# Performance work log

Hardware: AMD Instinct MI355X
Metric: run time of the kernel (lower is better)

## Reference

```python
import jax, jax.numpy as jnp
import numpy as np

B, TT, TA, H = 2, 128, 512, 1024
EPS = 1e-5


def _conv1d(x, w, b, pad):
    # x: [B, C_in, T], w: [C_out, C_in, K] -> [B, C_out, T]
    y = jax.lax.conv_general_dilated(x, w, window_strides=(1,), padding=[(pad, pad)],
                                     dimension_numbers=('NCH', 'OIH', 'NCH'))
    return y + b[None, :, None]


def _groupnorm1(x, g, b):
    # GroupNorm(num_groups=1): normalize over (C, T) per sample. x: [B, C, T]
    mu = jnp.mean(x, axis=(1, 2), keepdims=True)
    var = jnp.var(x, axis=(1, 2), keepdims=True)
    xn = (x - mu) * jax.lax.rsqrt(var + EPS)
    return xn * g[None, :, None] + b[None, :, None]


def setup_inputs() -> dict:
    key = jax.random.key(0)
    ks = jax.random.split(key, 16)
    s = 0.02
    return {
        'text_hidden': jax.random.normal(ks[0], (B, TT, H), jnp.float32),
        'audio_hidden': jax.random.normal(ks[1], (B, TA, H), jnp.float32),
        # alignment_proj: Linear(2H, H) -> ReLU -> Linear(H, 1)
        'a_w1': jax.random.normal(ks[2], (2 * H, H), jnp.float32) * s,
        'a_b1': jnp.zeros((H,), jnp.float32),
        'a_w2': jax.random.normal(ks[3], (H, 1), jnp.float32) * s,
        'a_b2': jnp.zeros((1,), jnp.float32),
        # duration_predictor: Conv1d(H,H,3) ReLU GN(1,H) Conv1d(H,H,3) ReLU GN(1,H) Conv1d(H,1,1)
        'd_w1': jax.random.normal(ks[4], (H, H, 3), jnp.float32) * s,
        'd_b1': jnp.zeros((H,), jnp.float32),
        'gn1_g': jnp.ones((H,), jnp.float32),
        'gn1_b': jnp.zeros((H,), jnp.float32),
        'd_w2': jax.random.normal(ks[5], (H, H, 3), jnp.float32) * s,
        'd_b2': jnp.zeros((H,), jnp.float32),
        'gn2_g': jnp.ones((H,), jnp.float32),
        'gn2_b': jnp.zeros((H,), jnp.float32),
        'd_w3': jax.random.normal(ks[6], (1, H, 1), jnp.float32) * s,
        'd_b3': jnp.zeros((1,), jnp.float32),
    }


def reference(text_hidden, audio_hidden, a_w1, a_b1, a_w2, a_b2,
              d_w1, d_b1, gn1_g, gn1_b, d_w2, d_b2, gn2_g, gn2_b, d_w3, d_b3):
    # ---- predict_durations ----
    x = jnp.swapaxes(text_hidden, 1, 2)                      # [B, H, TT]
    x = _groupnorm1(jax.nn.relu(_conv1d(x, d_w1, d_b1, 1)), gn1_g, gn1_b)
    x = _groupnorm1(jax.nn.relu(_conv1d(x, d_w2, d_b2, 1)), gn2_g, gn2_b)
    x = _conv1d(x, d_w3, d_b3, 0)                            # [B, 1, TT]
    durations = jax.nn.softplus(x[:, 0, :])                  # [B, TT]

    # ---- soft_mas (temperature = 1.0) ----
    # Linear on concat([text, audio]) == text @ W1[:H] + audio @ W1[H:] + b1
    t_part = jnp.einsum('bth,hd->btd', text_hidden, a_w1[:H])    # [B, TT, H]
    a_part = jnp.einsum('bah,hd->bad', audio_hidden, a_w1[H:])   # [B, TA, H]
    hid = jax.nn.relu(t_part[:, :, None, :] + a_part[:, None, :, :] + a_b1)  # [B,TT,TA,H]
    logits = jnp.einsum('btad,do->bta', hid, a_w2) + a_b2[0]     # [B, TT, TA]

    pos = jnp.arange(TA, dtype=logits.dtype)                     # audio positions j
    expected = jnp.arange(TT, dtype=logits.dtype) * (TA / TT)    # expected pos per text i
    monotonic_bias = -0.1 * jnp.abs(pos[None, :] - expected[:, None])  # [TT, TA]
    logits = logits + monotonic_bias[None, :, :]

    alignment = jax.nn.softmax(logits, axis=-1)
    return alignment, durations
```

## Files before the change

kernel.cpp:

```cpp
#include <hip/hip_runtime.h>
#include <hip/hip_bf16.h>


typedef __bf16 bf16_t;
typedef __bf16 bf16x8 __attribute__((ext_vector_type(8)));
typedef __bf16 bf16x4 __attribute__((ext_vector_type(4)));
typedef float  f32x4  __attribute__((ext_vector_type(4)));
typedef _Float16 f16_t;
typedef _Float16 f16x2 __attribute__((ext_vector_type(2)));
typedef _Float16 f16x4 __attribute__((ext_vector_type(4)));

#define EPSV 1e-5f

#define OFF_TEXTBF   0u
#define OFF_AUDIOBF  524288u
#define OFF_W1TOP    2621440u
#define OFF_W1BOT    4718592u
#define OFF_WC1      6815744u
#define OFF_WC2      13107200u
#define OFF_TP       19398656u
#define OFF_W2F      19922944u
#define OFF_APT      20447232u
#define OFF_XP0      22544384u
#define OFF_XP1      23076864u
#define OFF_Y2       23609344u
#define OFF_BST1     24133632u
#define OFF_BST2     24137728u
#define OFF_LP       24141824u

__global__ __launch_bounds__(256) void prep_k(
    const float* __restrict__ text, const float* __restrict__ audio,
    const float* __restrict__ w1,
    const float* __restrict__ w1c, const float* __restrict__ w2c,
    const float* __restrict__ w2,
    bf16_t* __restrict__ text_bf, bf16_t* __restrict__ xp0,
    bf16_t* __restrict__ audio_bf,
    bf16_t* __restrict__ topT, bf16_t* __restrict__ botT,
    bf16_t* __restrict__ wc1, bf16_t* __restrict__ wc2,
    bf16_t* __restrict__ xp1, f16_t* __restrict__ w2f)
{
    __shared__ float tile[32][33];
    const int bid = blockIdx.x;
    if (bid < 1280) {
        const int e = (bid * 256 + threadIdx.x) * 4;
        if (e < 262144) {
            float4 v = *(const float4*)&text[e];
            bf16x4 o; o[0] = (bf16_t)v.x; o[1] = (bf16_t)v.y; o[2] = (bf16_t)v.z; o[3] = (bf16_t)v.w;
            *(bf16x4*)&text_bf[e] = o;
            const int bt = e >> 10, h = e & 1023;
            const int b = bt >> 7, t = bt & 127;
            *(bf16x4*)&xp0[(size_t)(b * 130 + 1 + t) * 1024 + h] = o;
        } else {
            const int ea = e - 262144;
            float4 v = *(const float4*)&audio[ea];
            bf16x4 o; o[0] = (bf16_t)v.x; o[1] = (bf16_t)v.y; o[2] = (bf16_t)v.z; o[3] = (bf16_t)v.w;
            *(bf16x4*)&audio_bf[ea] = o;
        }
    } else if (bid < 3328) {
        const int b2 = bid - 1280;
        const int bx = b2 & 31, by = b2 >> 5;
        const int tx = threadIdx.x & 31, ty = threadIdx.x >> 5;
        #pragma unroll
        for (int j = 0; j < 4; ++j)
            tile[ty + j * 8][tx] = w1[(size_t)(by * 32 + ty + j * 8) * 1024 + bx * 32 + tx];
        __syncthreads();
        bf16_t* out = (by < 32) ? topT : botT;
        const int hbase = (by & 31) * 32;
        #pragma unroll
        for (int j = 0; j < 4; ++j) {
            const int d = bx * 32 + ty + j * 8;
            out[(size_t)d * 1024 + hbase + tx] = (bf16_t)tile[tx][ty + j * 8];
        }
    } else if (bid < 5376) {
        int b2 = bid - 3328;
        const float* w = (b2 < 1024) ? w1c : w2c;
        bf16_t* wc = (b2 < 1024) ? wc1 : wc2;
        b2 &= 1023;
        const int t = b2 * 256 + threadIdx.x;
        const int o = t >> 8, i4 = t & 255;
        const float* src = w + (size_t)o * 3072 + i4 * 12;
        float4 v0 = *(const float4*)&src[0];
        float4 v1 = *(const float4*)&src[4];
        float4 v2 = *(const float4*)&src[8];
        const float f[12] = {v0.x, v0.y, v0.z, v0.w, v1.x, v1.y, v1.z, v1.w, v2.x, v2.y, v2.z, v2.w};
        #pragma unroll
        for (int r = 0; r < 3; ++r) {
            bf16x4 o4;
            #pragma unroll
            for (int j = 0; j < 4; ++j) o4[j] = (bf16_t)f[j * 3 + r];
            *(bf16x4*)&wc[(size_t)r * 1048576 + (size_t)o * 1024 + i4 * 4] = o4;
        }
    } else {
        const int tid = threadIdx.x;
        const int rowmap[4] = {0, 129, 130, 259};
        const int f = tid * 16;
        const int r = f >> 10, w = f & 1023;
        bf16x8 z8 = (bf16x8)(bf16_t)0.0f;
        bf16_t* p0 = xp0 + (size_t)rowmap[r] * 1024 + w;
        bf16_t* p1 = xp1 + (size_t)rowmap[r] * 1024 + w;
        *(bf16x8*)p0 = z8; *(bf16x8*)(p0 + 8) = z8;
        *(bf16x8*)p1 = z8; *(bf16x8*)(p1 + 8) = z8;
        float4 wv = *(const float4*)&w2[tid * 4];
        f16x4 wo; wo[0] = (f16_t)wv.x; wo[1] = (f16_t)wv.y; wo[2] = (f16_t)wv.z; wo[3] = (f16_t)wv.w;
        *(f16x4*)&w2f[tid * 4] = wo;
    }
}

__device__ __forceinline__ void conv_tile(
    const bf16_t* __restrict__ Wc, const bf16_t* __restrict__ xp,
    const float* __restrict__ bias, bf16_t* __restrict__ out,
    int rowsPerB, int rowOff, float* __restrict__ bstat, int statIdx,
    int bx, int by, int tid, float* smem, float* sred, float* sredq)
{
    const int w = tid >> 6, l = tid & 63;
    const int bt0 = bx * 32, m0 = by * 16;
    const int i0 = w * 128;
    const int lm = l & 15, lk = (l >> 4) * 8;
    const int b = bt0 >> 7, tbase = bt0 & 127;
    f32x4 acc0 = (f32x4)(0.0f), acc1 = (f32x4)(0.0f);
    const bf16_t* aq = Wc + (size_t)(m0 + lm) * 1024 + i0 + lk;
    const bf16_t* bq = xp + (size_t)(b * 130 + tbase + lm) * 1024 + i0 + lk;
    #pragma unroll
    for (int r = 0; r < 3; ++r) {
        const bf16_t* ar = aq + (size_t)r * 1048576;
        const bf16_t* br = bq + (size_t)r * 1024;
        #pragma unroll
        for (int kk = 0; kk < 128; kk += 32) {
            bf16x8 af = *(const bf16x8*)(ar + kk);
            bf16x8 bf0 = *(const bf16x8*)(br + kk);
            bf16x8 bf1 = *(const bf16x8*)(br + 16384 + kk);
            acc0 = __builtin_amdgcn_mfma_f32_16x16x32_bf16(af, bf0, acc0, 0, 0, 0);
            acc1 = __builtin_amdgcn_mfma_f32_16x16x32_bf16(af, bf1, acc1, 0, 0, 0);
        }
    }
    {
        const int row = (l >> 4) * 4;
        #pragma unroll
        for (int r = 0; r < 4; ++r) {
            smem[w * 576 + (row + r) * 36 + lm] = acc0[r];
            smem[w * 576 + (row + r) * 36 + 16 + lm] = acc1[r];
        }
    }
    __syncthreads();
    const int m = tid >> 5, n = tid & 31;
    float v = 0.f;
    #pragma unroll
    for (int ww = 0; ww < 8; ++ww) v += smem[ww * 576 + m * 36 + n];
    v = fmaxf(v + bias[m0 + m], 0.f);
    float s = v, q = v * v;
    __syncthreads();
    smem[m * 36 + n] = v;
    #pragma unroll
    for (int off = 32; off > 0; off >>= 1) {
        s += __shfl_xor(s, off);
        q += __shfl_xor(q, off);
    }
    if (l == 0) { sred[w] = s; sredq[w] = q; }
    __syncthreads();
    if (tid == 0) {
        float ts = 0.f, tq = 0.f;
        #pragma unroll
        for (int ww = 0; ww < 8; ++ww) { ts += sred[ww]; tq += sredq[ww]; }
        bstat[statIdx * 2] = ts;
        bstat[statIdx * 2 + 1] = tq;
    }
    if (tid < 64) {
        const int row = tid >> 1, half = tid & 1;
        bf16x8 o8;
        #pragma unroll
        for (int j = 0; j < 8; ++j) o8[j] = (bf16_t)smem[(half * 8 + j) * 36 + row];
        const int t = tbase + row;
        *(bf16x8*)&out[(size_t)(b * rowsPerB + rowOff + t) * 1024 + m0 + half * 8] = o8;
    }
}

__device__ __forceinline__ void reduce_bstat(
    const float* __restrict__ bstat, int b, int tid,
    float* sr, float* sq, float& mu, float& rsig)
{
    const int lane = tid & 63, wid = tid >> 6;
    float s = 0.f, q = 0.f;
    if (tid < 256) {
        float2 v = ((const float2*)bstat)[b * 256 + tid];
        s = v.x; q = v.y;
    }
    #pragma unroll
    for (int off = 32; off > 0; off >>= 1) {
        s += __shfl_xor(s, off);
        q += __shfl_xor(q, off);
    }
    if (lane == 0) { sr[wid] = s; sq[wid] = q; }
    __syncthreads();
    float ts = 0.f, tq = 0.f;
    #pragma unroll
    for (int i = 0; i < 8; ++i) { ts += sr[i]; tq += sq[i]; }
    const float cnt = 131072.f;
    mu = ts / cnt;
    const float var = tq / cnt - mu * mu;
    rsig = rsqrtf(var + EPSV);
}

__device__ __forceinline__ void gemm_unit(
    int unit, int ut, float* base,
    const bf16_t* __restrict__ text_bf, const bf16_t* __restrict__ w1topT,
    const float* __restrict__ b1, f16_t* __restrict__ tp,
    const bf16_t* __restrict__ audio_bf, const bf16_t* __restrict__ w1botT,
    f16_t* __restrict__ apT4)
{
    const int is_tp = (unit < 256) ? 1 : 0;
    const int b2 = is_tp ? unit : unit - 256;
    const int n0 = (b2 & 31) * 32, m0 = (b2 >> 5) * 32;
    const int w = ut >> 6, l = ut & 63;
    const int lm = l & 15, lk = (l >> 4) * 8;
    const int k0 = w * 256;
    const bf16_t* A  = is_tp ? text_bf : audio_bf;
    const bf16_t* Bt = is_tp ? w1topT : w1botT;
    f32x4 acc[2][2];
    #pragma unroll
    for (int mt = 0; mt < 2; ++mt)
        #pragma unroll
        for (int nt = 0; nt < 2; ++nt) acc[mt][nt] = (f32x4)(0.0f);
    const bf16_t* Ap = A + (size_t)(m0 + lm) * 1024 + k0 + lk;
    const bf16_t* Bp = Bt + (size_t)(n0 + lm) * 1024 + k0 + lk;
    #pragma unroll
    for (int kk = 0; kk < 256; kk += 32) {
        bf16x8 af[2], bfr[2];
        #pragma unroll
        for (int i = 0; i < 2; ++i) af[i] = *(const bf16x8*)(Ap + (size_t)i * 16384 + kk);
        #pragma unroll
        for (int i = 0; i < 2; ++i) bfr[i] = *(const bf16x8*)(Bp + (size_t)i * 16384 + kk);
        #pragma unroll
        for (int mt = 0; mt < 2; ++mt)
            #pragma unroll
            for (int nt = 0; nt < 2; ++nt)
                acc[mt][nt] = __builtin_amdgcn_mfma_f32_16x16x32_bf16(af[mt], bfr[nt], acc[mt][nt], 0, 0, 0);
    }
    #pragma unroll
    for (int mt = 0; mt < 2; ++mt) {
        const int row = mt * 16 + (l >> 4) * 4;
        #pragma unroll
        for (int nt = 0; nt < 2; ++nt)
            #pragma unroll
            for (int r = 0; r < 4; ++r)
                base[w * 1152 + (row + r) * 36 + nt * 16 + lm] = acc[mt][nt][r];
    }
    __syncthreads();
    if (is_tp) {
        const int m = ut >> 3, n4 = (ut & 7) * 4;
        f16x4 v;
        #pragma unroll
        for (int j = 0; j < 4; ++j)
            v[j] = (f16_t)(base[m * 36 + n4 + j] + base[1152 + m * 36 + n4 + j]
                         + base[2304 + m * 36 + n4 + j] + base[3456 + m * 36 + n4 + j]
                         + b1[n0 + n4 + j]);
        *(f16x4*)&tp[(size_t)(m0 + m) * 1024 + n0 + n4] = v;
    } else {
        const int a = ut >> 3, q = ut & 7;
        const int b = m0 >> 9, a0 = m0 & 511;
        f16x4 v;
        #pragma unroll
        for (int c = 0; c < 4; ++c)
            v[c] = (f16_t)(base[a * 36 + q * 4 + c] + base[1152 + a * 36 + q * 4 + c]
                         + base[2304 + a * 36 + q * 4 + c] + base[3456 + a * 36 + q * 4 + c]);
        const size_t hq = (size_t)(n0 >> 2) + q;
        *(f16x4*)&apT4[(hq * 1024 + b * 512 + a0 + a) * 4] = v;
    }
}

__global__ __launch_bounds__(512, 4) void p2_k(
    const bf16_t* __restrict__ wc1, const bf16_t* __restrict__ xp0,
    const float* __restrict__ d_b1, bf16_t* __restrict__ xp1,
    float* __restrict__ bstat1,
    const bf16_t* __restrict__ text_bf, const bf16_t* __restrict__ w1topT,
    const float* __restrict__ a_b1, f16_t* __restrict__ tp,
    const bf16_t* __restrict__ audio_bf, const bf16_t* __restrict__ w1botT,
    f16_t* __restrict__ apT4)
{
    __shared__ float smem[9216];
    __shared__ float sred[8], sredq[8];
    const int bid = blockIdx.x;
    const int tid = threadIdx.x;
    if (bid < 512) {
        conv_tile(wc1, xp0, d_b1, xp1, 130, 1, bstat1, bid,
                  bid >> 6, bid & 63, tid, smem, sred, sredq);
    } else {
        const int unit = (bid - 512) * 2 + (tid >> 8);
        gemm_unit(unit, tid & 255, smem + (tid >> 8) * 4608,
                  text_bf, w1topT, a_b1, tp, audio_bf, w1botT, apT4);
    }
}

__device__ __forceinline__ float dot2_acc(f16x2 x, f16x2 w, float acc) {
#if __has_builtin(__builtin_amdgcn_fdot2)
    return __builtin_amdgcn_fdot2(x, w, acc, false);
#else
    return acc + (float)x[0] * (float)w[0] + (float)x[1] * (float)w[1];
#endif
}

__global__ __launch_bounds__(512) void p3_k(
    const f16_t* __restrict__ tp, const f16_t* __restrict__ apT4,
    const f16_t* __restrict__ w2f, float* __restrict__ lp,
    bf16_t* __restrict__ xp1, const float* __restrict__ bstat1,
    const float* __restrict__ g, const float* __restrict__ bet)
{
    __shared__ float sr[8], sq[8];
    const int bid = blockIdx.x;
    const int tid = threadIdx.x;
    if (bid < 256) {
        const int btp = bid & 63, hc = bid >> 6;
        const int bt0 = btp * 4;
        const int b = bt0 >> 7;
        const int a = tid;
        const f16_t* tpr = tp + (size_t)bt0 * 1024 + hc * 256;
        const f16_t* w2r = w2f + hc * 256;
        const f16_t* apc = apT4 + ((size_t)(hc * 64) * 1024 + b * 512 + a) * 4;
        float acc[4] = {0.f, 0.f, 0.f, 0.f};
        const f16x2 zero = (f16x2)(f16_t)0.0f;
        #pragma unroll 2
        for (int hq = 0; hq < 64; hq += 2) {
            f16x4 a0 = *(const f16x4*)(apc + (size_t)hq * 4096);
            f16x4 a1 = *(const f16x4*)(apc + (size_t)(hq + 1) * 4096);
            f16x4 w0 = *(const f16x4*)&w2r[hq * 4];
            f16x4 w1 = *(const f16x4*)&w2r[hq * 4 + 4];
            #pragma unroll
            for (int r = 0; r < 4; ++r) {
                f16x4 t0 = *(const f16x4*)&tpr[r * 1024 + hq * 4];
                f16x4 t1 = *(const f16x4*)&tpr[r * 1024 + hq * 4 + 4];
                f16x2 p;
                p = __builtin_elementwise_max((f16x2){t0[0] + a0[0], t0[1] + a0[1]}, zero);
                acc[r] = dot2_acc(p, (f16x2){w0[0], w0[1]}, acc[r]);
                p = __builtin_elementwise_max((f16x2){t0[2] + a0[2], t0[3] + a0[3]}, zero);
                acc[r] = dot2_acc(p, (f16x2){w0[2], w0[3]}, acc[r]);
                p = __builtin_elementwise_max((f16x2){t1[0] + a1[0], t1[1] + a1[1]}, zero);
                acc[r] = dot2_acc(p, (f16x2){w1[0], w1[1]}, acc[r]);
                p = __builtin_elementwise_max((f16x2){t1[2] + a1[2], t1[3] + a1[3]}, zero);
                acc[r] = dot2_acc(p, (f16x2){w1[2], w1[3]}, acc[r]);
            }
        }
        float* dst = lp + (size_t)(hc * 256 + bt0) * 512 + a;
        #pragma unroll
        for (int r = 0; r < 4; ++r) dst[(size_t)r * 512] = acc[r];
    } else {
        const int gb = bid - 256;
        const int b = (gb * 2) >> 7;
        float mu, rsig;
        reduce_bstat(bstat1, b, tid, sr, sq, mu, rsig);
        const int idx4 = gb * 512 + tid;
        const int e = idx4 * 4;
        const int bt = e >> 10, o = e & 1023;
        const int t = bt & 127;
        bf16_t* p = xp1 + (size_t)(b * 130 + 1 + t) * 1024 + o;
        bf16x4 v = *(bf16x4*)p;
        float4 gv = *(const float4*)&g[o];
        float4 bv = *(const float4*)&bet[o];
        bf16x4 ov;
        ov[0] = (bf16_t)(((float)v[0] - mu) * rsig * gv.x + bv.x);
        ov[1] = (bf16_t)(((float)v[1] - mu) * rsig * gv.y + bv.y);
        ov[2] = (bf16_t)(((float)v[2] - mu) * rsig * gv.z + bv.z);
        ov[3] = (bf16_t)(((float)v[3] - mu) * rsig * gv.w + bv.w);
        *(bf16x4*)p = ov;
    }
}

__global__ __launch_bounds__(512, 4) void conv2_k(
    const bf16_t* __restrict__ wc2, const bf16_t* __restrict__ xp1,
    const float* __restrict__ d_b2, bf16_t* __restrict__ y2,
    float* __restrict__ bstat2)
{
    __shared__ float smem[4608];
    __shared__ float sred[8], sredq[8];
    conv_tile(wc2, xp1, d_b2, y2, 128, 0, bstat2, blockIdx.x,
              blockIdx.x >> 6, blockIdx.x & 63, threadIdx.x, smem, sred, sredq);
}

__global__ __launch_bounds__(512) void combine_k(
    const float* __restrict__ lp, const float* __restrict__ b2,
    const bf16_t* __restrict__ y2, const float* __restrict__ bstat2,
    const float* __restrict__ g, const float* __restrict__ bet,
    const float* __restrict__ w3, const float* __restrict__ b3,
    float* __restrict__ out)
{
    __shared__ float redm[8], redsum[8];
    const int bid = blockIdx.x;
    const int tid = threadIdx.x;
    if (bid < 256) {
        const int bt = bid, t = bt & 127;
        const int a = tid;
        const int lane = a & 63, wid = a >> 6;
        const size_t base = (size_t)bt * 512 + a;
        float v = lp[base] + lp[131072 + base] + lp[262144 + base] + lp[393216 + base];
        v += b2[0] - 0.1f * fabsf((float)a - 4.0f * (float)t);
        float m = v;
        #pragma unroll
        for (int off = 32; off > 0; off >>= 1) m = fmaxf(m, __shfl_xor(m, off));
        if (lane == 0) redm[wid] = m;
        __syncthreads();
        float M = redm[0];
        #pragma unroll
        for (int i = 1; i < 8; ++i) M = fmaxf(M, redm[i]);
        const float e = expf(v - M);
        float s = e;
        #pragma unroll
        for (int off = 32; off > 0; off >>= 1) s += __shfl_xor(s, off);
        if (lane == 0) redsum[wid] = s;
        __syncthreads();
        float S = redsum[0];
        #pragma unroll
        for (int i = 1; i < 8; ++i) S += redsum[i];
        out[(size_t)bt * 512 + a] = e * (1.0f / S);
    } else {
        const int cb = bid - 256;
        const int b = (cb * 8) >> 7;
        float mu, rsig;
        reduce_bstat(bstat2, b, tid, redm, redsum, mu, rsig);
        const int lane = tid & 63, w = tid >> 6;
        const int bt = cb * 8 + w;
        const bf16_t* row = y2 + (size_t)bt * 1024 + lane * 16;
        float s1 = 0.f, s2 = 0.f, s3 = 0.f;
        #pragma unroll
        for (int c = 0; c < 2; ++c) {
            bf16x8 yv = *(const bf16x8*)(row + c * 8);
            #pragma unroll
            for (int j = 0; j < 8; ++j) {
                const int i = lane * 16 + c * 8 + j;
                const float gw = g[i] * w3[i];
                s1 += gw * (float)yv[j];
                s2 += gw;
                s3 += bet[i] * w3[i];
            }
        }
        #pragma unroll
        for (int off = 32; off > 0; off >>= 1) {
            s1 += __shfl_xor(s1, off);
            s2 += __shfl_xor(s2, off);
            s3 += __shfl_xor(s3, off);
        }
        if (lane == 0) {
            const float t = rsig * (s1 - mu * s2) + s3 + b3[0];
            out[131072 + bt] = fmaxf(t, 0.f) + log1pf(expf(-fabsf(t)));
        }
    }
}

extern "C" void kernel_launch(void* const* d_in, const int* in_sizes, int n_in,
                              void* d_out, int out_size, void* d_ws, size_t ws_size,
                              hipStream_t stream) {
    const float* text   = (const float*)d_in[0];
    const float* audio  = (const float*)d_in[1];
    const float* a_w1   = (const float*)d_in[2];
    const float* a_b1   = (const float*)d_in[3];
    const float* a_w2   = (const float*)d_in[4];
    const float* a_b2   = (const float*)d_in[5];
    const float* d_w1   = (const float*)d_in[6];
    const float* d_b1   = (const float*)d_in[7];
    const float* gn1_g  = (const float*)d_in[8];
    const float* gn1_b  = (const float*)d_in[9];
    const float* d_w2   = (const float*)d_in[10];
    const float* d_b2   = (const float*)d_in[11];
    const float* gn2_g  = (const float*)d_in[12];
    const float* gn2_b  = (const float*)d_in[13];
    const float* d_w3   = (const float*)d_in[14];
    const float* d_b3   = (const float*)d_in[15];

    char* ws = (char*)d_ws;
    float* outf = (float*)d_out;

    bf16_t* text_bf  = (bf16_t*)(ws + OFF_TEXTBF);
    bf16_t* audio_bf = (bf16_t*)(ws + OFF_AUDIOBF);
    bf16_t* w1topT   = (bf16_t*)(ws + OFF_W1TOP);
    bf16_t* w1botT   = (bf16_t*)(ws + OFF_W1BOT);
    bf16_t* wc1      = (bf16_t*)(ws + OFF_WC1);
    bf16_t* wc2      = (bf16_t*)(ws + OFF_WC2);
    f16_t*  tp       = (f16_t*) (ws + OFF_TP);
    f16_t*  w2f      = (f16_t*) (ws + OFF_W2F);
    f16_t*  apT4     = (f16_t*) (ws + OFF_APT);
    bf16_t* xp0      = (bf16_t*)(ws + OFF_XP0);
    bf16_t* xp1      = (bf16_t*)(ws + OFF_XP1);
    bf16_t* y2       = (bf16_t*)(ws + OFF_Y2);
    float*  bstat1   = (float*) (ws + OFF_BST1);
    float*  bstat2   = (float*) (ws + OFF_BST2);
    float*  lp       = (float*) (ws + OFF_LP);

    prep_k<<<dim3(5377), 256, 0, stream>>>(text, audio, a_w1, d_w1, d_w2, a_w2,
                                           text_bf, xp0, audio_bf, w1topT, w1botT,
                                           wc1, wc2, xp1, w2f);
    p2_k<<<dim3(1152), 512, 0, stream>>>(wc1, xp0, d_b1, xp1, bstat1,
                                         text_bf, w1topT, a_b1, tp,
                                         audio_bf, w1botT, apT4);
    p3_k<<<dim3(384), 512, 0, stream>>>(tp, apT4, w2f, lp,
                                        xp1, bstat1, gn1_g, gn1_b);
    conv2_k<<<dim3(512), 512, 0, stream>>>(wc2, xp1, d_b2, y2, bstat2);
    combine_k<<<dim3(288), 512, 0, stream>>>(lp, a_b2, y2, bstat2,
                                             gn2_g, gn2_b, d_w3, d_b3, outf);
}
```

Baseline: 184.0 us.

## Fold GroupNorm1 into conv2 weights and merge conv2 into logits kernel

GroupNorm1's affine scale is folded into the conv2 weights during prep, along with per-output-channel weight sums. The normalization is then applied algebraically in the conv2 epilogue (rsig*acc + Sb - mu*rsig*Sg, with boundary corrections at the padded edges), so the separate pass that rewrote xp1 in place is gone. Because conv2 no longer waits on that pass, it runs in the same launch as the alignment-logit blocks, cutting one kernel launch and one read-modify-write of xp1. The trade-off is that conv2 now runs on un-normalized bf16 activations, which may shift rounding, and mu/rsig are reduced redundantly in every conv2 block.

Measured after the change: 181.6 us. Within noise of the previous version (-1.3%).

```diff
diff --git a/kernel.cpp b/kernel.cpp
--- a/kernel.cpp
+++ b/kernel.cpp
@@ -27,17 +27,21 @@
 #define OFF_BST1     24133632u
 #define OFF_BST2     24137728u
 #define OFF_LP       24141824u
+#define OFF_SG       26238976u
+#define OFF_SB       26251264u
 
 __global__ __launch_bounds__(256) void prep_k(
     const float* __restrict__ text, const float* __restrict__ audio,
     const float* __restrict__ w1,
     const float* __restrict__ w1c, const float* __restrict__ w2c,
     const float* __restrict__ w2,
+    const float* __restrict__ g1, const float* __restrict__ b1g,
     bf16_t* __restrict__ text_bf, bf16_t* __restrict__ xp0,
     bf16_t* __restrict__ audio_bf,
     bf16_t* __restrict__ topT, bf16_t* __restrict__ botT,
     bf16_t* __restrict__ wc1, bf16_t* __restrict__ wc2,
-    bf16_t* __restrict__ xp1, f16_t* __restrict__ w2f)
+    bf16_t* __restrict__ xp1, f16_t* __restrict__ w2f,
+    float* __restrict__ Sg, float* __restrict__ Sb)
 {
     __shared__ float tile[32][33];
     const int bid = blockIdx.x;
@@ -73,22 +77,62 @@
         }
     } else if (bid < 5376) {
         int b2 = bid - 3328;
-        const float* w = (b2 < 1024) ? w1c : w2c;
-        bf16_t* wc = (b2 < 1024) ? wc1 : wc2;
+        const int is2 = (b2 >= 1024) ? 1 : 0;
+        const float* w = is2 ? w2c : w1c;
+        bf16_t* wc = is2 ? wc2 : wc1;
         b2 &= 1023;
-        const int t = b2 * 256 + threadIdx.x;
-        const int o = t >> 8, i4 = t & 255;
+        const int o = b2, i4 = threadIdx.x;
         const float* src = w + (size_t)o * 3072 + i4 * 12;
         float4 v0 = *(const float4*)&src[0];
         float4 v1 = *(const float4*)&src[4];
         float4 v2 = *(const float4*)&src[8];
         const float f[12] = {v0.x, v0.y, v0.z, v0.w, v1.x, v1.y, v1.z, v1.w, v2.x, v2.y, v2.z, v2.w};
+        float g4[4] = {1.f, 1.f, 1.f, 1.f}, bb4[4] = {0.f, 0.f, 0.f, 0.f};
+        if (is2) {
+            float4 gv = *(const float4*)&g1[i4 * 4];
+            float4 bv = *(const float4*)&b1g[i4 * 4];
+            g4[0] = gv.x; g4[1] = gv.y; g4[2] = gv.z; g4[3] = gv.w;
+            bb4[0] = bv.x; bb4[1] = bv.y; bb4[2] = bv.z; bb4[3] = bv.w;
+        }
+        float sgr[3] = {0.f, 0.f, 0.f}, sbr[3] = {0.f, 0.f, 0.f};
         #pragma unroll
         for (int r = 0; r < 3; ++r) {
             bf16x4 o4;
             #pragma unroll
-            for (int j = 0; j < 4; ++j) o4[j] = (bf16_t)f[j * 3 + r];
+            for (int j = 0; j < 4; ++j) {
+                const float wv = f[j * 3 + r];
+                const float ws = wv * g4[j];
+                sgr[r] += ws;
+                sbr[r] += wv * bb4[j];
+                o4[j] = (bf16_t)(is2 ? ws : wv);
+            }
             *(bf16x4*)&wc[(size_t)r * 1048576 + (size_t)o * 1024 + i4 * 4] = o4;
+        }
+        if (is2) {
+            #pragma unroll
+            for (int off = 32; off > 0; off >>= 1) {
+                #pragma unroll
+                for (int r = 0; r < 3; ++r) {
+                    sgr[r] += __shfl_xor(sgr[r], off);
+                    sbr[r] += __shfl_xor(sbr[r], off);
+                }
+            }
+            float* red = &tile[0][0];
+            const int wid = threadIdx.x >> 6, lane = threadIdx.x & 63;
+            if (lane == 0) {
+                #pragma unroll
+                for (int r = 0; r < 3; ++r) {
+                    red[wid * 6 + r] = sgr[r];
+                    red[wid * 6 + 3 + r] = sbr[r];
+                }
+            }
+            __syncthreads();
+            if (threadIdx.x < 6) {
+                const float v = red[threadIdx.x] + red[6 + threadIdx.x]
+                              + red[12 + threadIdx.x] + red[18 + threadIdx.x];
+                if (threadIdx.x < 3) Sg[o * 3 + threadIdx.x] = v;
+                else                 Sb[o * 3 + threadIdx.x - 3] = v;
+            }
         }
     } else {
         const int tid = threadIdx.x;
@@ -200,6 +244,85 @@
     rsig = rsqrtf(var + EPSV);
 }
 
+__device__ __forceinline__ void conv2_tile(
+    const bf16_t* __restrict__ Wc, const bf16_t* __restrict__ xp,
+    const float* __restrict__ bias, bf16_t* __restrict__ out,
+    const float* __restrict__ bstat1,
+    const float* __restrict__ Sg, const float* __restrict__ Sb,
+    float* __restrict__ bstat2, int statIdx,
+    int bx, int by, int tid, float* smem, float* sred, float* sredq,
+    float* sr, float* sq)
+{
+    const int w = tid >> 6, l = tid & 63;
+    const int bt0 = bx * 32, m0 = by * 16;
+    const int i0 = w * 128;
+    const int lm = l & 15, lk = (l >> 4) * 8;
+    const int b = bt0 >> 7, tbase = bt0 & 127;
+    float mu1, rsig1;
+    reduce_bstat(bstat1, b, tid, sr, sq, mu1, rsig1);
+    f32x4 acc0 = (f32x4)(0.0f), acc1 = (f32x4)(0.0f);
+    const bf16_t* aq = Wc + (size_t)(m0 + lm) * 1024 + i0 + lk;
+    const bf16_t* bq = xp + (size_t)(b * 130 + tbase + lm) * 1024 + i0 + lk;
+    #pragma unroll
+    for (int r = 0; r < 3; ++r) {
+        const bf16_t* ar = aq + (size_t)r * 1048576;
+        const bf16_t* br = bq + (size_t)r * 1024;
+        #pragma unroll
+        for (int kk = 0; kk < 128; kk += 32) {
+            bf16x8 af = *(const bf16x8*)(ar + kk);
+            bf16x8 bf0 = *(const bf16x8*)(br + kk);
+            bf16x8 bf1 = *(const bf16x8*)(br + 16384 + kk);
+            acc0 = __builtin_amdgcn_mfma_f32_16x16x32_bf16(af, bf0, acc0, 0, 0, 0);
+            acc1 = __builtin_amdgcn_mfma_f32_16x16x32_bf16(af, bf1, acc1, 0, 0, 0);
+        }
+    }
+    {
+        const int row = (l >> 4) * 4;
+        #pragma unroll
+        for (int r = 0; r < 4; ++r) {
+            smem[w * 576 + (row + r) * 36 + lm] = acc0[r];
+            smem[w * 576 + (row + r) * 36 + 16 + lm] = acc1[r];
+        }
+    }
+    __syncthreads();
+    const int m = tid >> 5, n = tid & 31;
+    float v = 0.f;
+    #pragma unroll
+    for (int ww = 0; ww < 8; ++ww) v += smem[ww * 576 + m * 36 + n];
+    const int o = m0 + m;
+    const int tloc = tbase + n;
+    float sb = Sb[o * 3] + Sb[o * 3 + 1] + Sb[o * 3 + 2];
+    float sg = Sg[o * 3] + Sg[o * 3 + 1] + Sg[o * 3 + 2];
+    if (tloc == 0)   { sb -= Sb[o * 3];     sg -= Sg[o * 3]; }
+    if (tloc == 127) { sb -= Sb[o * 3 + 2]; sg -= Sg[o * 3 + 2]; }
+    v = fmaxf(rsig1 * v + sb - mu1 * rsig1 * sg + bias[o], 0.f);
+    float s = v, q = v * v;
+    __syncthreads();
+    smem[m * 36 + n] = v;
+    #pragma unroll
+    for (int off = 32; off > 0; off >>= 1) {
+        s += __shfl_xor(s, off);
+        q += __shfl_xor(q, off);
+    }
+    if (l == 0) { sred[w] = s; sredq[w] = q; }
+    __syncthreads();
+    if (tid == 0) {
+        float ts = 0.f, tq = 0.f;
+        #pragma unroll
+        for (int ww = 0; ww < 8; ++ww) { ts += sred[ww]; tq += sredq[ww]; }
+        bstat2[statIdx * 2] = ts;
+        bstat2[statIdx * 2 + 1] = tq;
+    }
+    if (tid < 64) {
+        const int row = tid >> 1, half = tid & 1;
+        bf16x8 o8;
+        #pragma unroll
+        for (int j = 0; j < 8; ++j) o8[j] = (bf16_t)smem[(half * 8 + j) * 36 + row];
+        const int t = tbase + row;
+        *(bf16x8*)&out[(size_t)(b * 128 + t) * 1024 + m0 + half * 8] = o8;
+    }
+}
+
 __device__ __forceinline__ void gemm_unit(
     int unit, int ut, float* base,
     const bf16_t* __restrict__ text_bf, const bf16_t* __restrict__ w1topT,
@@ -298,17 +421,24 @@
 #endif
 }
 
-__global__ __launch_bounds__(512) void p3_k(
+__global__ __launch_bounds__(512, 4) void p3_k(
+    const bf16_t* __restrict__ wc2, const bf16_t* __restrict__ xp1,
+    const float* __restrict__ d_b2, bf16_t* __restrict__ y2,
+    float* __restrict__ bstat2, const float* __restrict__ bstat1,
+    const float* __restrict__ Sg, const float* __restrict__ Sb,
     const f16_t* __restrict__ tp, const f16_t* __restrict__ apT4,
-    const f16_t* __restrict__ w2f, float* __restrict__ lp,
-    bf16_t* __restrict__ xp1, const float* __restrict__ bstat1,
-    const float* __restrict__ g, const float* __restrict__ bet)
-{
-    __shared__ float sr[8], sq[8];
+    const f16_t* __restrict__ w2f, float* __restrict__ lp)
+{
+    __shared__ float smem[4608];
+    __shared__ float sred[8], sredq[8], sr[8], sq[8];
     const int bid = blockIdx.x;
     const int tid = threadIdx.x;
-    if (bid < 256) {
-        const int btp = bid & 63, hc = bid >> 6;
+    if (bid < 512) {
+        conv2_tile(wc2, xp1, d_b2, y2, bstat1, Sg, Sb, bstat2, bid,
+                   bid >> 6, bid & 63, tid, smem, sred, sredq, sr, sq);
+    } else {
+        const int lb = bid - 512;
+        const int btp = lb & 63, hc = lb >> 6;
         const int bt0 = btp * 4;
         const int b = bt0 >> 7;
         const int a = tid;
@@ -341,37 +471,7 @@
         float* dst = lp + (size_t)(hc * 256 + bt0) * 512 + a;
         #pragma unroll
         for (int r = 0; r < 4; ++r) dst[(size_t)r * 512] = acc[r];
-    } else {
-        const int gb = bid - 256;
-        const int b = (gb * 2) >> 7;
-        float mu, rsig;
-        reduce_bstat(bstat1, b, tid, sr, sq, mu, rsig);
-        const int idx4 = gb * 512 + tid;
-        const int e = idx4 * 4;
-        const int bt = e >> 10, o = e & 1023;
-        const int t = bt & 127;
-        bf16_t* p = xp1 + (size_t)(b * 130 + 1 + t) * 1024 + o;
-        bf16x4 v = *(bf16x4*)p;
-        float4 gv = *(const float4*)&g[o];
-        float4 bv = *(const float4*)&bet[o];
-        bf16x4 ov;
-        ov[0] = (bf16_t)(((float)v[0] - mu) * rsig * gv.x + bv.x);
-        ov[1] = (bf16_t)(((float)v[1] - mu) * rsig * gv.y + bv.y);
-        ov[2] = (bf16_t)(((float)v[2] - mu) * rsig * gv.z + bv.z);
-        ov[3] = (bf16_t)(((float)v[3] - mu) * rsig * gv.w + bv.w);
-        *(bf16x4*)p = ov;
-    }
-}
-
-__global__ __launch_bounds__(512, 4) void conv2_k(
-    const bf16_t* __restrict__ wc2, const bf16_t* __restrict__ xp1,
-    const float* __restrict__ d_b2, bf16_t* __restrict__ y2,
-    float* __restrict__ bstat2)
-{
-    __shared__ float smem[4608];
-    __shared__ float sred[8], sredq[8];
-    conv_tile(wc2, xp1, d_b2, y2, 128, 0, bstat2, blockIdx.x,
-              blockIdx.x >> 6, blockIdx.x & 63, threadIdx.x, smem, sred, sredq);
+    }
 }
 
 __global__ __launch_bounds__(512) void combine_k(
@@ -481,16 +581,18 @@
     float*  bstat1   = (float*) (ws + OFF_BST1);
     float*  bstat2   = (float*) (ws + OFF_BST2);
     float*  lp       = (float*) (ws + OFF_LP);
+    float*  Sgp      = (float*) (ws + OFF_SG);
+    float*  Sbp      = (float*) (ws + OFF_SB);
 
     prep_k<<<dim3(5377), 256, 0, stream>>>(text, audio, a_w1, d_w1, d_w2, a_w2,
+                                           gn1_g, gn1_b,
                                            text_bf, xp0, audio_bf, w1topT, w1botT,
-                                           wc1, wc2, xp1, w2f);
+                                           wc1, wc2, xp1, w2f, Sgp, Sbp);
     p2_k<<<dim3(1152), 512, 0, stream>>>(wc1, xp0, d_b1, xp1, bstat1,
                                          text_bf, w1topT, a_b1, tp,
                                          audio_bf, w1botT, apT4);
-    p3_k<<<dim3(384), 512, 0, stream>>>(tp, apT4, w2f, lp,
-                                        xp1, bstat1, gn1_g, gn1_b);
-    conv2_k<<<dim3(512), 512, 0, stream>>>(wc2, xp1, d_b2, y2, bstat2);
+    p3_k<<<dim3(768), 512, 0, stream>>>(wc2, xp1, d_b2, y2, bstat2, bstat1,
+                                        Sgp, Sbp, tp, apT4, w2f, lp);
     combine_k<<<dim3(288), 512, 0, stream>>>(lp, a_b2, y2, bstat2,
                                              gn2_g, gn2_b, d_w3, d_b3, outf);
 }
```
